# Performance work log

Hardware: AMD Instinct MI355X
Metric: run time of the kernel (lower is better)

Reference implementation:

```python
import jax, jax.numpy as jnp
import numpy as np

NEG = -1000000000.0

def setup_inputs() -> dict:
    key = jax.random.key(0)
    k1, k2 = jax.random.split(key)
    b, t, d, k = 32, 4096, 512, 8
    h = jax.random.normal(k1, (b, t, d), dtype=jnp.float32)
    mask = jnp.ones((b, t), dtype=bool)
    queries = jax.random.normal(k2, (k, d), dtype=jnp.float32)
    return {"h": h, "mask": mask, "queries": queries}

def reference(h, mask, queries):
    # attn scores: (b, k, t), no scaling
    attn = jnp.einsum('kd,btd->bkt', queries, h)
    attn = jnp.where(mask[:, None, :], attn, NEG)
    attn = jax.nn.softmax(attn, axis=-1)
    slots = jnp.einsum('bkt,btd->bkd', attn, h)
    return slots
```

## Files before the change

### kernel.cpp

```cpp
#include <hip/hip_runtime.h>
#include <hip/hip_bf16.h>


#define NEGV -1000000000.0f

constexpr int B = 32;
constexpr int T = 4096;
constexpr int D = 512;
constexpr int K = 8;
constexpr float SHIFT = 80.0f;

typedef unsigned int u32x2 __attribute__((ext_vector_type(2)));

__device__ __forceinline__ float rdlane(float v, int l) {
  return __uint_as_float(__builtin_amdgcn_readlane(__float_as_uint(v), l));
}

__device__ __forceinline__ void pl32swap(float& a, float& b) {
  u32x2 r = __builtin_amdgcn_permlane32_swap(
      __float_as_uint(a), __float_as_uint(b), false, false);
  a = __uint_as_float(r[0]);
  b = __uint_as_float(r[1]);
}

__device__ __forceinline__ void pl16swap(float& a, float& b) {
  u32x2 r = __builtin_amdgcn_permlane16_swap(
      __float_as_uint(a), __float_as_uint(b), false, false);
  a = __uint_as_float(r[0]);
  b = __uint_as_float(r[1]);
}

template <int CTRL>
__device__ __forceinline__ float dppmov(float x) {
  return __uint_as_float(__builtin_amdgcn_update_dpp(
      __float_as_uint(x), __float_as_uint(x), CTRL, 0xF, 0xF, true));
}

__device__ __forceinline__ void load_row(const float* __restrict__ hb,
                                         const int* __restrict__ mb, int t,
                                         int tend, float (&hv)[8], int& mk) {
  const int tt = (t < tend) ? t : (tend - 1);
  const float4 a = *(const float4*)(hb + (size_t)tt * D);
  const float4 c = *(const float4*)(hb + (size_t)tt * D + 4);
  hv[0] = a.x; hv[1] = a.y; hv[2] = a.z; hv[3] = a.w;
  hv[4] = c.x; hv[5] = c.y; hv[6] = c.z; hv[7] = c.w;
  mk = mb[tt];
}

__device__ __forceinline__ void compute_row(const float (&hv)[8], int mk,
                                            const float (&qv)[4][8],
                                            float (&acc)[4][8],
                                            float& llane) {
  float v0 = 0.f, v1 = 0.f, v2 = 0.f, v3 = 0.f;
#pragma unroll
  for (int j = 0; j < 8; ++j) {
    v0 = fmaf(qv[0][j], hv[j], v0);
    v1 = fmaf(qv[1][j], hv[j], v1);
    v2 = fmaf(qv[2][j], hv[j], v2);
    v3 = fmaf(qv[3][j], hv[j], v3);
  }

  pl32swap(v0, v2); float u02 = v0 + v2;
  pl32swap(v1, v3); float u13 = v1 + v3;
  pl16swap(u02, u13); float y = u02 + u13;
  y += dppmov<0x128>(y);
  y += dppmov<0xB1>(y);
  y += dppmov<0x4E>(y);
  y += dppmov<0x141>(y);

  const float s = mk ? y : NEGV;
  const float el = __expf(s - SHIFT);
  llane += el;

  const float e0 = rdlane(el, 0),  e1 = rdlane(el, 16);
  const float e2 = rdlane(el, 32), e3 = rdlane(el, 48);
#pragma unroll
  for (int j = 0; j < 8; ++j) {
    acc[0][j] = fmaf(e0, hv[j], acc[0][j]);
    acc[1][j] = fmaf(e1, hv[j], acc[1][j]);
    acc[2][j] = fmaf(e2, hv[j], acc[2][j]);
    acc[3][j] = fmaf(e3, hv[j], acc[3][j]);
  }
}

__global__ __launch_bounds__(512, 4) void pool_pass1(
    const float* __restrict__ h, const int* __restrict__ mask,
    const float* __restrict__ q, float* __restrict__ wsacc,
    float* __restrict__ wsl, int nchunks, int rows) {
  const int chunk = blockIdx.x;
  const int b = blockIdx.y;
  const int tid = threadIdx.x;
  const int wave = tid >> 6;
  const int lane = tid & 63;
  const int sg = wave & 1;
  const int qtr = wave >> 1;
  const int dbase = lane * 8;
  const int rowsw = rows >> 2;
  const int t0 = chunk * rows + qtr * rowsw;
  const int tend = t0 + rowsw;

  float qv[4][8];
#pragma unroll
  for (int ss = 0; ss < 4; ++ss) {
    const float* qp = q + (size_t)(sg * 4 + ss) * D + dbase;
    const float4 a = *(const float4*)(qp);
    const float4 c = *(const float4*)(qp + 4);
    qv[ss][0]=a.x; qv[ss][1]=a.y; qv[ss][2]=a.z; qv[ss][3]=a.w;
    qv[ss][4]=c.x; qv[ss][5]=c.y; qv[ss][6]=c.z; qv[ss][7]=c.w;
  }

  float acc[4][8] = {};
  float llane = 0.f;

  const float* hb = h + (size_t)b * T * D + dbase;
  const int* mb = mask + (size_t)b * T;

  float hv0[8], hv1[8], hv2[8], hv3[8];
  int mk0, mk1, mk2, mk3;

  load_row(hb, mb, t0 + 0, tend, hv0, mk0);
  load_row(hb, mb, t0 + 1, tend, hv1, mk1);
  load_row(hb, mb, t0 + 2, tend, hv2, mk2);
  for (int g = 0; g < rowsw; g += 4) {
    load_row(hb, mb, t0 + g + 3, tend, hv3, mk3);
    compute_row(hv0, mk0, qv, acc, llane);
    load_row(hb, mb, t0 + g + 4, tend, hv0, mk0);
    compute_row(hv1, mk1, qv, acc, llane);
    load_row(hb, mb, t0 + g + 5, tend, hv1, mk1);
    compute_row(hv2, mk2, qv, acc, llane);
    load_row(hb, mb, t0 + g + 6, tend, hv2, mk2);
    compute_row(hv3, mk3, qv, acc, llane);
  }

  float l[4];
#pragma unroll
  for (int ss = 0; ss < 4; ++ss) l[ss] = rdlane(llane, 16 * ss);

  __shared__ float so[3][2][4][D];
  __shared__ float sl[3][2][4];
  if (qtr != 0) {
#pragma unroll
    for (int ss = 0; ss < 4; ++ss) {
      float4 o;
      o.x=acc[ss][0]; o.y=acc[ss][1]; o.z=acc[ss][2]; o.w=acc[ss][3];
      *(float4*)(&so[qtr - 1][sg][ss][dbase]) = o;
      o.x=acc[ss][4]; o.y=acc[ss][5]; o.z=acc[ss][6]; o.w=acc[ss][7];
      *(float4*)(&so[qtr - 1][sg][ss][dbase + 4]) = o;
    }
    if (lane < 4) sl[qtr - 1][sg][lane] = l[lane];
  }
  __syncthreads();
  if (qtr == 0) {
    size_t pbase = ((size_t)(b * nchunks + chunk) * K + sg * 4);
#pragma unroll
    for (int ss = 0; ss < 4; ++ss) {
      float* ap = wsacc + (pbase + ss) * D + dbase;
      float4 o;
#pragma unroll
      for (int j = 0; j < 4; ++j) {
        float r = acc[ss][j] + so[0][sg][ss][dbase + j] +
                  so[1][sg][ss][dbase + j] + so[2][sg][ss][dbase + j];
        (&o.x)[j] = r;
      }
      *(float4*)(ap) = o;
#pragma unroll
      for (int j = 0; j < 4; ++j) {
        float r = acc[ss][4 + j] + so[0][sg][ss][dbase + 4 + j] +
                  so[1][sg][ss][dbase + 4 + j] + so[2][sg][ss][dbase + 4 + j];
        (&o.x)[j] = r;
      }
      *(float4*)(ap + 4) = o;
    }
    if (lane < 4)
      wsl[pbase + lane] =
          l[lane] + sl[0][sg][lane] + sl[1][sg][lane] + sl[2][sg][lane];
  }
}

__global__ __launch_bounds__(256) void pool_pass2(
    const float* __restrict__ wsacc, const float* __restrict__ wsl,
    float* __restrict__ out, int nchunks) {
  const int bk = blockIdx.x;
  const int tid = threadIdx.x;
  const int wave = tid >> 6;
  const int lane = tid & 63;
  const int b = bk >> 3;
  const int k = bk & 7;

  __shared__ float so[4][D];
  __shared__ float sl[4];

  float o[8] = {0,0,0,0,0,0,0,0};
  float lsum = 0.f;
  for (int c = wave; c < nchunks; c += 4) {
    size_t idx = (size_t)(b * nchunks + c) * K + k;
    const float* ap = wsacc + idx * D + lane * 8;
    float4 a0 = *(const float4*)(ap);
    float4 a1 = *(const float4*)(ap + 4);
    o[0] += a0.x; o[1] += a0.y; o[2] += a0.z; o[3] += a0.w;
    o[4] += a1.x; o[5] += a1.y; o[6] += a1.z; o[7] += a1.w;
    lsum += wsl[idx];
  }
#pragma unroll
  for (int j = 0; j < 8; ++j) so[wave][lane * 8 + j] = o[j];
  if (lane == 0) sl[wave] = lsum;
  __syncthreads();

  const float L = sl[0] + sl[1] + sl[2] + sl[3];
  const float inv = 1.0f / L;
  const int d2 = tid * 2;
  float r0 = so[0][d2] + so[1][d2] + so[2][d2] + so[3][d2];
  float r1 = so[0][d2 + 1] + so[1][d2 + 1] + so[2][d2 + 1] + so[3][d2 + 1];
  float2 v;
  v.x = r0 * inv;
  v.y = r1 * inv;
  *(float2*)(out + (size_t)bk * D + d2) = v;
}

extern "C" void kernel_launch(void* const* d_in, const int* in_sizes, int n_in,
                              void* d_out, int out_size, void* d_ws, size_t ws_size,
                              hipStream_t stream) {
  const float* h = (const float*)d_in[0];
  const int* mask = (const int*)d_in[1];
  const float* q = (const float*)d_in[2];
  float* out = (float*)d_out;

  int nc = 16;
  while (nc > 1 &&
         (size_t)B * nc * K * (D + 1) * sizeof(float) > ws_size)
    nc >>= 1;

  float* wsacc = (float*)d_ws;
  float* wsl = wsacc + (size_t)B * nc * K * D;

  dim3 g1(nc, B);
  pool_pass1<<<g1, 512, 0, stream>>>(h, mask, q, wsacc, wsl, nc, T / nc);
  pool_pass2<<<B * K, 256, 0, stream>>>(wsacc, wsl, out, nc);
}
```

Baseline: 57.32 us.

## Fuse chunk reduction into pass1 via last-block atomic counter

```diff
diff --git a/kernel.cpp b/kernel.cpp
--- a/kernel.cpp
+++ b/kernel.cpp
@@ -83,10 +83,11 @@
   }
 }
 
-__global__ __launch_bounds__(512, 4) void pool_pass1(
+__global__ __launch_bounds__(512, 4) void pool_fused(
     const float* __restrict__ h, const int* __restrict__ mask,
     const float* __restrict__ q, float* __restrict__ wsacc,
-    float* __restrict__ wsl, int nchunks, int rows) {
+    float* __restrict__ wsl, int* __restrict__ cnt,
+    float* __restrict__ out, int nchunks, int rows) {
   const int chunk = blockIdx.x;
   const int b = blockIdx.y;
   const int tid = threadIdx.x;
@@ -174,47 +175,38 @@
     if (lane < 4)
       wsl[pbase + lane] =
           l[lane] + sl[0][sg][lane] + sl[1][sg][lane] + sl[2][sg][lane];
-  }
-}
-
-__global__ __launch_bounds__(256) void pool_pass2(
-    const float* __restrict__ wsacc, const float* __restrict__ wsl,
-    float* __restrict__ out, int nchunks) {
-  const int bk = blockIdx.x;
-  const int tid = threadIdx.x;
-  const int wave = tid >> 6;
-  const int lane = tid & 63;
-  const int b = bk >> 3;
-  const int k = bk & 7;
-
-  __shared__ float so[4][D];
-  __shared__ float sl[4];
-
-  float o[8] = {0,0,0,0,0,0,0,0};
-  float lsum = 0.f;
-  for (int c = wave; c < nchunks; c += 4) {
-    size_t idx = (size_t)(b * nchunks + c) * K + k;
-    const float* ap = wsacc + idx * D + lane * 8;
-    float4 a0 = *(const float4*)(ap);
-    float4 a1 = *(const float4*)(ap + 4);
-    o[0] += a0.x; o[1] += a0.y; o[2] += a0.z; o[3] += a0.w;
-    o[4] += a1.x; o[5] += a1.y; o[6] += a1.z; o[7] += a1.w;
-    lsum += wsl[idx];
-  }
-#pragma unroll
-  for (int j = 0; j < 8; ++j) so[wave][lane * 8 + j] = o[j];
-  if (lane == 0) sl[wave] = lsum;
+    __threadfence();
+  }
   __syncthreads();
 
-  const float L = sl[0] + sl[1] + sl[2] + sl[3];
-  const float inv = 1.0f / L;
-  const int d2 = tid * 2;
-  float r0 = so[0][d2] + so[1][d2] + so[2][d2] + so[3][d2];
-  float r1 = so[0][d2 + 1] + so[1][d2 + 1] + so[2][d2 + 1] + so[3][d2 + 1];
-  float2 v;
-  v.x = r0 * inv;
-  v.y = r1 * inv;
-  *(float2*)(out + (size_t)bk * D + d2) = v;
+  __shared__ int lastflag;
+  if (tid == 0) {
+    int old = atomicAdd(&cnt[b], 1);
+    lastflag = (old == nchunks - 1) ? 1 : 0;
+  }
+  __syncthreads();
+  if (lastflag) {
+    __threadfence();
+    const int k = wave;
+    float o[8] = {0,0,0,0,0,0,0,0};
+    float lsum = 0.f;
+    for (int c = 0; c < nchunks; ++c) {
+      const size_t idx = (size_t)(b * nchunks + c) * K + k;
+      const float* ap = wsacc + idx * D + dbase;
+      const float4 a0 = *(const float4*)(ap);
+      const float4 a1 = *(const float4*)(ap + 4);
+      o[0] += a0.x; o[1] += a0.y; o[2] += a0.z; o[3] += a0.w;
+      o[4] += a1.x; o[5] += a1.y; o[6] += a1.z; o[7] += a1.w;
+      lsum += wsl[idx];
+    }
+    const float inv = 1.0f / lsum;
+    float* op = out + ((size_t)b * K + k) * D + dbase;
+    float4 v;
+    v.x = o[0]*inv; v.y = o[1]*inv; v.z = o[2]*inv; v.w = o[3]*inv;
+    *(float4*)(op) = v;
+    v.x = o[4]*inv; v.y = o[5]*inv; v.z = o[6]*inv; v.w = o[7]*inv;
+    *(float4*)(op + 4) = v;
+  }
 }
 
 extern "C" void kernel_launch(void* const* d_in, const int* in_sizes, int n_in,
@@ -227,13 +219,17 @@
 
   int nc = 16;
   while (nc > 1 &&
-         (size_t)B * nc * K * (D + 1) * sizeof(float) > ws_size)
+         (size_t)B * nc * K * (D + 1) * sizeof(float) + 128 + B * 4 > ws_size)
     nc >>= 1;
 
   float* wsacc = (float*)d_ws;
   float* wsl = wsacc + (size_t)B * nc * K * D;
+  size_t cnt_off = ((size_t)B * nc * K * (D + 1) * sizeof(float) + 127) & ~(size_t)127;
+  int* cnt = (int*)((char*)d_ws + cnt_off);
+
+  hipMemsetAsync(cnt, 0, B * sizeof(int), stream);
 
   dim3 g1(nc, B);
-  pool_pass1<<<g1, 512, 0, stream>>>(h, mask, q, wsacc, wsl, nc, T / nc);
-  pool_pass2<<<B * K, 256, 0, stream>>>(wsacc, wsl, out, nc);
-}
+  pool_fused<<<g1, 512, 0, stream>>>(h, mask, q, wsacc, wsl, cnt, out, nc,
+                                     T / nc);
+}
```

Measured after the change: 141.2 us. 146% more time.
